# Kernel optimization log

Measured on AMD Instinct MI355X. Metric: run time of the kernel, lower is better.

## Reference

```python
import math
import jax, jax.numpy as jnp
import numpy as np

B, H, S, D = 2, 16, 2048, 64
NEG = -1000000000.0


def setup_inputs() -> dict:
    key = jax.random.key(0)
    kq, kk, kv = jax.random.split(key, 3)
    q = jax.random.normal(kq, (B, H, S, D), dtype=jnp.float32)
    k = jax.random.normal(kk, (B, H, S, D), dtype=jnp.float32)
    v = jax.random.normal(kv, (B, H, S, D), dtype=jnp.float32)
    attention_mask = jnp.ones((B, S), dtype=jnp.float32)
    return {"q": q, "k": k, "v": v, "attention_mask": attention_mask}


def reference(q, k, v, attention_mask):
    head_dim = q.shape[-1]
    scaling = 1.0 / math.sqrt(head_dim)
    # scores: [B, H, S, S]
    scores = jnp.einsum("bhqd,bhkd->bhqk", q, k) * scaling
    seq_len = q.shape[-2]
    # causal mask: upper triangle (excluding diag) gets large negative
    causal_mask = jnp.triu(jnp.full((seq_len, seq_len), NEG, dtype=scores.dtype), k=1)
    scores = scores + causal_mask[None, None, :, :]
    # additive attention mask: [B,1,1,S]
    add_mask = (1.0 - attention_mask)[:, None, None, :] * NEG
    scores = scores + add_mask
    weights = jax.nn.softmax(scores, axis=-1)  # dropout p=0.0 -> identity
    out = jnp.einsum("bhqk,bhkd->bhqd", weights, v)
    return out
```

## Files before the change

kernel.cpp:

```cpp
#include <hip/hip_runtime.h>

typedef _Float16 half8 __attribute__((ext_vector_type(8)));
typedef float f32x4 __attribute__((ext_vector_type(4)));

#define MFMA_F16 __builtin_amdgcn_mfma_f32_16x16x32_f16

constexpr int Bc = 2, Hc = 16, Sc = 2048, Dc = 64;
constexpr int QBLK = 128, KVBLK = 64;
constexpr float LOG2E = 1.4426950408889634f;
constexpr float SCALE_LOG2E = 0.125f * LOG2E;
constexpr float NEGBIG = -1.0e9f;

constexpr size_t WS_KIMG = 524288;
constexpr size_t WS_VIMG = WS_KIMG + (size_t)32 * 32 * 8192;

#define J(q, a, b) ((uint32_t)(q) | ((uint32_t)(a) << 8) | ((uint32_t)(b) << 16))
__device__ const uint32_t JOBS[40] = {
    J(15,0,8),  J(15,8,16), J(15,16,24), J(15,24,32),
    J(14,7,15), J(14,22,30),J(11,0,8),   J(11,8,16),
    J(13,0,7),  J(14,15,22),J(14,0,7),   J(3,0,8),
    J(7,8,16),  J(7,0,8),   J(10,14,22), J(11,16,24),
    J(13,7,14), J(13,14,21),J(13,21,28), J(12,6,13),
    J(12,19,26),J(10,0,7),  J(10,7,14),  J(9,6,13),
    J(9,13,20), J(6,0,7),   J(6,7,14),   J(12,0,6),
    J(12,13,19),J(9,0,6),   J(8,0,6),    J(8,6,12),
    J(8,12,18), J(5,0,6),   J(5,6,12),   J(2,0,6),
    J(4,0,5),   J(4,5,10),  J(1,0,4),    J(0,0,2)
};

__global__ __launch_bounds__(256, 4)
void prep(const float* __restrict__ K, const float* __restrict__ V,
          const float* __restrict__ AM, float* __restrict__ O,
          float* __restrict__ ws)
{
    const int bid = blockIdx.x;
    const int t   = threadIdx.x;

    if (bid >= 1024) {
        const int zb = bid - 1024;
        float4* O4 = (float4*)O;
        const float4 z = {0.f, 0.f, 0.f, 0.f};
        #pragma unroll
        for (int i = 0; i < 4; ++i) O4[(size_t)zb * 1024 + i * 256 + t] = z;
        if (zb < 16) {
            float4* L4 = (float4*)ws;
            #pragma unroll
            for (int i = 0; i < 4; ++i) L4[(size_t)zb * 1024 + i * 256 + t] = z;
        }
        return;
    }

    __shared__ float Vlds[64][65];
    const int bh  = bid & 31;
    const int kvt = bid >> 5;
    const size_t base = (size_t)bh * Sc * Dc + (size_t)kvt * KVBLK * Dc;
    _Float16* Kimg = (_Float16*)((char*)ws + WS_KIMG) + ((size_t)(bh * 32 + kvt) << 12);
    _Float16* Vimg = (_Float16*)((char*)ws + WS_VIMG) + ((size_t)(bh * 32 + kvt) << 12);

    #pragma unroll
    for (int i = 0; i < 4; ++i) {
        const int r = (t >> 4) + 16 * i, c = (t & 15) * 4;
        float4 v = *(const float4*)(V + base + (size_t)r * Dc + c);
        Vlds[r][c] = v.x; Vlds[r][c+1] = v.y; Vlds[r][c+2] = v.z; Vlds[r][c+3] = v.w;
    }

    {
        const int kv = t >> 2;
        const float* krow = K + base + (size_t)kv * Dc;
        #pragma unroll
        for (int pp = 0; pp < 2; ++pp) {
            const int pg = (t & 3) * 2 + pp;
            const int g  = pg ^ (kv & 7);
            float4 a = *(const float4*)(krow + g * 8);
            float4 b = *(const float4*)(krow + g * 8 + 4);
            half8 h = { (_Float16)a.x, (_Float16)a.y, (_Float16)a.z, (_Float16)a.w,
                        (_Float16)b.x, (_Float16)b.y, (_Float16)b.z, (_Float16)b.w };
            *(half8*)(Kimg + kv * 64 + pg * 8) = h;
        }
    }
    __syncthreads();

    {
        const int d = t >> 2;
        #pragma unroll
        for (int pp = 0; pp < 2; ++pp) {
            const int pg = (t & 3) * 2 + pp;
            const int g  = pg ^ (d & 7);
            half8 h;
            #pragma unroll
            for (int e = 0; e < 8; ++e) {
                const int key = ((g >> 2) << 5) | ((e >> 2) << 4) | ((g & 3) << 2) | (e & 3);
                h[e] = (_Float16)Vlds[key][d];
            }
            *(half8*)(Vimg + d * 64 + pg * 8) = h;
        }
    }

    if ((bh & 15) == 0 && t < 64) {
        const size_t idx = (size_t)(bh >> 4) * Sc + kvt * 64 + t;
        (ws + 65536)[idx] = (1.0f - AM[idx]) * (NEGBIG * LOG2E);
    }
}

__global__ __launch_bounds__(256, 4)
void sdpa_p1(const float* __restrict__ Q, float* __restrict__ Oacc,
             float* __restrict__ ws)
{
    __shared__ _Float16 KhL[2][4096];
    __shared__ _Float16 VtL[2][4096];

    const float* maddp = ws + 65536;
    const _Float16* Kimg = (const _Float16*)((const char*)ws + WS_KIMG);
    const _Float16* Vimg = (const _Float16*)((const char*)ws + WS_VIMG);
    float* Lp = ws;

    const int bid = blockIdx.x;
    const int bh  = bid & 31;
    const uint32_t job = JOBS[bid >> 5];
    const int qt  = job & 255;
    const int kv0 = (job >> 8) & 255;
    const int kv1 = (job >> 16) & 255;
    const int b   = bh >> 4;
    const int qb  = qt * QBLK;

    const int t    = threadIdx.x;
    const int w    = t >> 6;
    const int lane = t & 63;
    const int l16  = lane & 15;
    const int hi   = lane >> 4;
    const int hi4  = hi * 4;

    const size_t base  = (size_t)bh * Sc * Dc;
    const size_t tbase = (size_t)bh * 32;

    half8 kst[2], vst[2];
    auto stage_load = [&](int kvt_) {
        const _Float16* kg = Kimg + ((tbase + kvt_) << 12) + t * 8;
        const _Float16* vg = Vimg + ((tbase + kvt_) << 12) + t * 8;
        kst[0] = *(const half8*)kg;
        kst[1] = *(const half8*)(kg + 2048);
        vst[0] = *(const half8*)vg;
        vst[1] = *(const half8*)(vg + 2048);
    };
    auto stage_write = [&](int bf) {
        *(half8*)(&KhL[bf][t * 8])        = kst[0];
        *(half8*)(&KhL[bf][t * 8 + 2048]) = kst[1];
        *(half8*)(&VtL[bf][t * 8])        = vst[0];
        *(half8*)(&VtL[bf][t * 8 + 2048]) = vst[1];
    };

    half8 qfrag[2][2];
    #pragma unroll
    for (int g = 0; g < 2; ++g) {
        const float* qp = Q + base + (size_t)(qb + w * 32 + g * 16 + l16) * Dc + hi * 8;
        #pragma unroll
        for (int cc = 0; cc < 2; ++cc) {
            float4 x0 = *(const float4*)(qp + cc * 32);
            float4 x1 = *(const float4*)(qp + cc * 32 + 4);
            qfrag[g][cc] = (half8){
                (_Float16)(x0.x * SCALE_LOG2E), (_Float16)(x0.y * SCALE_LOG2E),
                (_Float16)(x0.z * SCALE_LOG2E), (_Float16)(x0.w * SCALE_LOG2E),
                (_Float16)(x1.x * SCALE_LOG2E), (_Float16)(x1.y * SCALE_LOG2E),
                (_Float16)(x1.z * SCALE_LOG2E), (_Float16)(x1.w * SCALE_LOG2E) };
        }
    }

    f32x4 o[2][4];
    #pragma unroll
    for (int g = 0; g < 2; ++g)
        #pragma unroll
        for (int dt = 0; dt < 4; ++dt) o[g][dt] = (f32x4){0.f, 0.f, 0.f, 0.f};
    float lacc[2] = {0.f, 0.f};

    stage_load(kv0);
    stage_write(0);
    __syncthreads();

    for (int kvt = kv0; kvt < kv1; ++kvt) {
        const int  cur  = (kvt - kv0) & 1;
        const bool pref = (kvt + 1 < kv1);
        if (pref) stage_load(kvt + 1);
        const int kvb = kvt * KVBLK;

        f32x4 st[2][4];
        #pragma unroll
        for (int g = 0; g < 2; ++g)
            #pragma unroll
            for (int nt = 0; nt < 4; ++nt) st[g][nt] = (f32x4){0.f, 0.f, 0.f, 0.f};
        #pragma unroll
        for (int nt = 0; nt < 4; ++nt) {
            const int row = nt * 16 + l16;
            const int rsw = row & 7;
            #pragma unroll
            for (int cc = 0; cc < 2; ++cc) {
                const half8 kf = *(const half8*)(&KhL[cur][row * 64 + (((cc << 2) | hi) ^ rsw) * 8]);
                #pragma unroll
                for (int g = 0; g < 2; ++g)
                    st[g][nt] = MFMA_F16(kf, qfrag[g][cc], st[g][nt], 0, 0, 0);
            }
        }

        #pragma unroll
        for (int nt = 0; nt < 4; ++nt) {
            const f32x4 mr = *(const f32x4*)(maddp + (size_t)b * Sc + kvb + nt * 16 + hi4);
            #pragma unroll
            for (int g = 0; g < 2; ++g)
                #pragma unroll
                for (int r = 0; r < 4; ++r) st[g][nt][r] += mr[r];
        }
        if (kvt >= 2 * qt) {
            #pragma unroll
            for (int g = 0; g < 2; ++g) {
                const int qrow = qb + w * 32 + g * 16 + l16;
                #pragma unroll
                for (int nt = 0; nt < 4; ++nt)
                    #pragma unroll
                    for (int r = 0; r < 4; ++r)
                        if (kvb + nt * 16 + hi4 + r > qrow) st[g][nt][r] = NEGBIG;
            }
        }

        #pragma unroll
        for (int g = 0; g < 2; ++g)
            #pragma unroll
            for (int nt = 0; nt < 4; ++nt)
                #pragma unroll
                for (int r = 0; r < 4; ++r) {
                    const float p = exp2f(st[g][nt][r]);
                    lacc[g] += p;
                    st[g][nt][r] = p;
                }

        half8 pa[2][2];
        #pragma unroll
        for (int g = 0; g < 2; ++g)
            #pragma unroll
            for (int cc = 0; cc < 2; ++cc)
                #pragma unroll
                for (int jj = 0; jj < 8; ++jj)
                    pa[g][cc][jj] = (_Float16)st[g][2 * cc + (jj >> 2)][jj & 3];

        #pragma unroll
        for (int dt = 0; dt < 4; ++dt) {
            const int row = dt * 16 + l16;
            const int rsw = row & 7;
            #pragma unroll
            for (int cc = 0; cc < 2; ++cc) {
                const half8 vf = *(const half8*)(&VtL[cur][row * 64 + (((cc << 2) | hi) ^ rsw) * 8]);
                #pragma unroll
                for (int g = 0; g < 2; ++g)
                    o[g][dt] = MFMA_F16(pa[g][cc], vf, o[g][dt], 0, 0, 0);
            }
        }

        if (pref) stage_write(cur ^ 1);
        __syncthreads();
    }

    #pragma unroll
    for (int g = 0; g < 2; ++g) {
        float la = lacc[g];
        la += __shfl_xor(la, 16);
        la += __shfl_xor(la, 32);
        if (hi == 0)
            unsafeAtomicAdd(&Lp[(size_t)bh * Sc + qb + w * 32 + g * 16 + l16], la);
        float* op = Oacc + base + (size_t)(qb + w * 32 + g * 16 + hi4) * Dc + l16;
        #pragma unroll
        for (int r = 0; r < 4; ++r)
            #pragma unroll
            for (int dt = 0; dt < 4; ++dt)
                unsafeAtomicAdd(&op[(size_t)r * Dc + dt * 16], o[g][dt][r]);
    }
}

__global__ __launch_bounds__(256)
void sdpa_norm(float* __restrict__ O, const float* __restrict__ L)
{
    const int i = blockIdx.x * 256 + threadIdx.x;
    float4* o4 = (float4*)O;
    float4 v = o4[i];
    const float inv = 1.0f / L[i >> 4];
    v.x *= inv; v.y *= inv; v.z *= inv; v.w *= inv;
    o4[i] = v;
}

extern "C" void kernel_launch(void* const* d_in, const int* in_sizes, int n_in,
                              void* d_out, int out_size, void* d_ws, size_t ws_size,
                              hipStream_t stream)
{
    const float* q  = (const float*)d_in[0];
    const float* k  = (const float*)d_in[1];
    const float* v  = (const float*)d_in[2];
    const float* am = (const float*)d_in[3];
    float* out = (float*)d_out;
    float* wsf = (float*)d_ws;

    prep    <<<2048, 256, 0, stream>>>(k, v, am, out, wsf);
    sdpa_p1 <<<1280, 256, 0, stream>>>(q, out, wsf);
    sdpa_norm<<<4096, 256, 0, stream>>>(out, wsf);
}
```

Baseline: 174.9 us.

## Load pre-arranged MFMA fragments directly from global memory, dropping LDS staging

The prep kernel now writes K and V fp16 images in exact per-lane MFMA fragment order, so each wave can read its operands with contiguous 16-byte global loads. The attention kernel drops its double-buffered LDS staging and the per-tile __syncthreads, loading K and V fragments straight into registers. The aim is to remove LDS traffic and block-level barriers. In exchange, each of the 4 waves reads the same tile from global/L2 separately, which adds load volume and exposes latency without explicit prefetch, and register pressure goes up.

```diff
diff --git a/kernel.cpp b/kernel.cpp
--- a/kernel.cpp
+++ b/kernel.cpp
@@ -5,14 +5,15 @@
 
 #define MFMA_F16 __builtin_amdgcn_mfma_f32_16x16x32_f16
 
-constexpr int Bc = 2, Hc = 16, Sc = 2048, Dc = 64;
+constexpr int Sc = 2048, Dc = 64;
 constexpr int QBLK = 128, KVBLK = 64;
 constexpr float LOG2E = 1.4426950408889634f;
 constexpr float SCALE_LOG2E = 0.125f * LOG2E;
 constexpr float NEGBIG = -1.0e9f;
 
+constexpr size_t WS_MADD = 65536;
 constexpr size_t WS_KIMG = 524288;
-constexpr size_t WS_VIMG = WS_KIMG + (size_t)32 * 32 * 8192;
+constexpr size_t WS_VIMG = WS_KIMG + (size_t)1024 * 8192;
 
 #define J(q, a, b) ((uint32_t)(q) | ((uint32_t)(a) << 8) | ((uint32_t)(b) << 16))
 __device__ const uint32_t JOBS[40] = {
@@ -64,41 +65,38 @@
         Vlds[r][c] = v.x; Vlds[r][c+1] = v.y; Vlds[r][c+2] = v.z; Vlds[r][c+3] = v.w;
     }
 
-    {
-        const int kv = t >> 2;
-        const float* krow = K + base + (size_t)kv * Dc;
-        #pragma unroll
-        for (int pp = 0; pp < 2; ++pp) {
-            const int pg = (t & 3) * 2 + pp;
-            const int g  = pg ^ (kv & 7);
-            float4 a = *(const float4*)(krow + g * 8);
-            float4 b = *(const float4*)(krow + g * 8 + 4);
-            half8 h = { (_Float16)a.x, (_Float16)a.y, (_Float16)a.z, (_Float16)a.w,
-                        (_Float16)b.x, (_Float16)b.y, (_Float16)b.z, (_Float16)b.w };
-            *(half8*)(Kimg + kv * 64 + pg * 8) = h;
-        }
+    #pragma unroll
+    for (int ss = 0; ss < 2; ++ss) {
+        const int s = t + 256 * ss;
+        const int nt = s >> 7, cc = (s >> 6) & 1, hi = (s >> 4) & 3, l16 = s & 15;
+        const float* kp = K + base + (size_t)(nt * 16 + l16) * Dc + cc * 32 + hi * 8;
+        float4 a = *(const float4*)kp;
+        float4 b = *(const float4*)(kp + 4);
+        half8 h = { (_Float16)a.x, (_Float16)a.y, (_Float16)a.z, (_Float16)a.w,
+                    (_Float16)b.x, (_Float16)b.y, (_Float16)b.z, (_Float16)b.w };
+        *(half8*)(Kimg + (size_t)s * 8) = h;
     }
     __syncthreads();
 
-    {
-        const int d = t >> 2;
-        #pragma unroll
-        for (int pp = 0; pp < 2; ++pp) {
-            const int pg = (t & 3) * 2 + pp;
-            const int g  = pg ^ (d & 7);
-            half8 h;
-            #pragma unroll
-            for (int e = 0; e < 8; ++e) {
-                const int key = ((g >> 2) << 5) | ((e >> 2) << 4) | ((g & 3) << 2) | (e & 3);
-                h[e] = (_Float16)Vlds[key][d];
-            }
-            *(half8*)(Vimg + d * 64 + pg * 8) = h;
-        }
+    #pragma unroll
+    for (int ss = 0; ss < 2; ++ss) {
+        const int s = t + 256 * ss;
+        const int dt = s >> 7, cc = (s >> 6) & 1, hi = (s >> 4) & 3, l16 = s & 15;
+        const int d = dt * 16 + l16;
+        half8 h;
+        #pragma unroll
+        for (int j = 0; j < 8; ++j) {
+            const int ks  = cc * 32 + hi * 8 + j;
+            const int key = ((ks >> 5) << 5) | (((ks >> 2) & 1) << 4)
+                          | (((ks >> 3) & 3) << 2) | (ks & 3);
+            h[j] = (_Float16)Vlds[key][d];
+        }
+        *(half8*)(Vimg + (size_t)s * 8) = h;
     }
 
     if ((bh & 15) == 0 && t < 64) {
         const size_t idx = (size_t)(bh >> 4) * Sc + kvt * 64 + t;
-        (ws + 65536)[idx] = (1.0f - AM[idx]) * (NEGBIG * LOG2E);
+        (ws + WS_MADD)[idx] = (1.0f - AM[idx]) * (NEGBIG * LOG2E);
     }
 }
 
@@ -106,10 +104,7 @@
 void sdpa_p1(const float* __restrict__ Q, float* __restrict__ Oacc,
              float* __restrict__ ws)
 {
-    __shared__ _Float16 KhL[2][4096];
-    __shared__ _Float16 VtL[2][4096];
-
-    const float* maddp = ws + 65536;
+    const float* maddp = ws + WS_MADD;
     const _Float16* Kimg = (const _Float16*)((const char*)ws + WS_KIMG);
     const _Float16* Vimg = (const _Float16*)((const char*)ws + WS_VIMG);
     float* Lp = ws;
@@ -133,22 +128,6 @@
     const size_t base  = (size_t)bh * Sc * Dc;
     const size_t tbase = (size_t)bh * 32;
 
-    half8 kst[2], vst[2];
-    auto stage_load = [&](int kvt_) {
-        const _Float16* kg = Kimg + ((tbase + kvt_) << 12) + t * 8;
-        const _Float16* vg = Vimg + ((tbase + kvt_) << 12) + t * 8;
-        kst[0] = *(const half8*)kg;
-        kst[1] = *(const half8*)(kg + 2048);
-        vst[0] = *(const half8*)vg;
-        vst[1] = *(const half8*)(vg + 2048);
-    };
-    auto stage_write = [&](int bf) {
-        *(half8*)(&KhL[bf][t * 8])        = kst[0];
-        *(half8*)(&KhL[bf][t * 8 + 2048]) = kst[1];
-        *(half8*)(&VtL[bf][t * 8])        = vst[0];
-        *(half8*)(&VtL[bf][t * 8 + 2048]) = vst[1];
-    };
-
     half8 qfrag[2][2];
     #pragma unroll
     for (int g = 0; g < 2; ++g) {
@@ -172,33 +151,31 @@
         for (int dt = 0; dt < 4; ++dt) o[g][dt] = (f32x4){0.f, 0.f, 0.f, 0.f};
     float lacc[2] = {0.f, 0.f};
 
-    stage_load(kv0);
-    stage_write(0);
-    __syncthreads();
-
     for (int kvt = kv0; kvt < kv1; ++kvt) {
-        const int  cur  = (kvt - kv0) & 1;
-        const bool pref = (kvt + 1 < kv1);
-        if (pref) stage_load(kvt + 1);
+        const _Float16* Kt = Kimg + ((tbase + kvt) << 12) + lane * 8;
+        const _Float16* Vt = Vimg + ((tbase + kvt) << 12) + lane * 8;
         const int kvb = kvt * KVBLK;
 
+        half8 kf[8];
+        #pragma unroll
+        for (int i = 0; i < 8; ++i) kf[i] = *(const half8*)(Kt + i * 512);
+
         f32x4 st[2][4];
         #pragma unroll
         for (int g = 0; g < 2; ++g)
             #pragma unroll
             for (int nt = 0; nt < 4; ++nt) st[g][nt] = (f32x4){0.f, 0.f, 0.f, 0.f};
         #pragma unroll
-        for (int nt = 0; nt < 4; ++nt) {
-            const int row = nt * 16 + l16;
-            const int rsw = row & 7;
-            #pragma unroll
-            for (int cc = 0; cc < 2; ++cc) {
-                const half8 kf = *(const half8*)(&KhL[cur][row * 64 + (((cc << 2) | hi) ^ rsw) * 8]);
+        for (int nt = 0; nt < 4; ++nt)
+            #pragma unroll
+            for (int cc = 0; cc < 2; ++cc)
                 #pragma unroll
                 for (int g = 0; g < 2; ++g)
-                    st[g][nt] = MFMA_F16(kf, qfrag[g][cc], st[g][nt], 0, 0, 0);
-            }
-        }
+                    st[g][nt] = MFMA_F16(kf[nt * 2 + cc], qfrag[g][cc], st[g][nt], 0, 0, 0);
+
+        half8 vfA[4];
+        #pragma unroll
+        for (int i = 0; i < 4; ++i) vfA[i] = *(const half8*)(Vt + i * 512);
 
         #pragma unroll
         for (int nt = 0; nt < 4; ++nt) {
@@ -240,21 +217,24 @@
                 for (int jj = 0; jj < 8; ++jj)
                     pa[g][cc][jj] = (_Float16)st[g][2 * cc + (jj >> 2)][jj & 3];
 
-        #pragma unroll
-        for (int dt = 0; dt < 4; ++dt) {
-            const int row = dt * 16 + l16;
-            const int rsw = row & 7;
-            #pragma unroll
-            for (int cc = 0; cc < 2; ++cc) {
-                const half8 vf = *(const half8*)(&VtL[cur][row * 64 + (((cc << 2) | hi) ^ rsw) * 8]);
+        half8 vfB[4];
+        #pragma unroll
+        for (int i = 0; i < 4; ++i) vfB[i] = *(const half8*)(Vt + (4 + i) * 512);
+
+        #pragma unroll
+        for (int dt = 0; dt < 2; ++dt)
+            #pragma unroll
+            for (int cc = 0; cc < 2; ++cc)
                 #pragma unroll
                 for (int g = 0; g < 2; ++g)
-                    o[g][dt] = MFMA_F16(pa[g][cc], vf, o[g][dt], 0, 0, 0);
-            }
-        }
-
-        if (pref) stage_write(cur ^ 1);
-        __syncthreads();
+                    o[g][dt] = MFMA_F16(pa[g][cc], vfA[dt * 2 + cc], o[g][dt], 0, 0, 0);
+        #pragma unroll
+        for (int dt = 2; dt < 4; ++dt)
+            #pragma unroll
+            for (int cc = 0; cc < 2; ++cc)
+                #pragma unroll
+                for (int g = 0; g < 2; ++g)
+                    o[g][dt] = MFMA_F16(pa[g][cc], vfB[(dt - 2) * 2 + cc], o[g][dt], 0, 0, 0);
     }
 
     #pragma unroll
```

New measurement: 171.1 us. -2.1%, faster.
